# Kernel optimization log

Measured on AMD Instinct MI355X. Metric: run time of the kernel, lower is better.

Reference implementation:

```python
import jax, jax.numpy as jnp
import numpy as np

N, C, CI, H, W = 64, 512, 256, 12, 4
EPS = 1e-5


def _conv1x1(v, w, b=None):
    # v: [n, cin, h, w], w: [cout, cin]
    o = jnp.einsum('nchw,oc->nohw', v, w)
    if b is not None:
        o = o + b[None, :, None, None]
    return o


def _layernorm(v, g, b):
    # normalize over (C, H, W) per sample, affine params shaped [C, H, W]
    mu = v.mean(axis=(1, 2, 3), keepdims=True)
    var = v.var(axis=(1, 2, 3), keepdims=True)
    return (v - mu) / jnp.sqrt(var + EPS) * g[None] + b[None]


def setup_inputs() -> dict:
    key = jax.random.key(0)
    ks = jax.random.split(key, 12)
    s = 0.02
    return {
        'x': jax.random.normal(ks[0], (N, C, H, W), dtype=jnp.float32),
        'theta_w': jax.random.normal(ks[1], (CI, C), dtype=jnp.float32) * s,
        'theta_b': jnp.zeros((CI,), dtype=jnp.float32),
        'phi_w': jax.random.normal(ks[2], (CI, C), dtype=jnp.float32) * s,
        'phi_b': jnp.zeros((CI,), dtype=jnp.float32),
        'conv1_w': jax.random.normal(ks[3], (C, C), dtype=jnp.float32) * s,
        'conv2_w': jax.random.normal(ks[4], (C, C), dtype=jnp.float32) * s,
        'ln1_g': jnp.ones((C, H, W), dtype=jnp.float32),
        'ln1_b': jnp.zeros((C, H, W), dtype=jnp.float32),
        'ln2_g': jnp.ones((C, H, W), dtype=jnp.float32),
        'ln2_b': jnp.zeros((C, H, W), dtype=jnp.float32),
    }


def reference(x, theta_w, theta_b, phi_w, phi_b, conv1_w, conv2_w,
              ln1_g, ln1_b, ln2_g, ln2_b):
    n = x.shape[0]
    hw = H * W
    # 1x1 conv projections (conv is per-sample, so compute once on the N nodes
    # instead of on the N^2 gathered copies -- identical math)
    theta = _conv1x1(x, theta_w, theta_b)          # [N, CI, H, W]  (gallery proj)
    phi = _conv1x1(x, phi_w, phi_b)                # [N, CI, H, W]  (query proj)
    # MaxPool2d(2,2) on phi -> [N, CI, 6, 2] -> [N, CI, 12]
    phi_p = phi.reshape(n, CI, H // 2, 2, W // 2, 2).max(axis=(3, 5))
    phi_p = phi_p.reshape(n, CI, -1)               # [N, CI, 12]
    t = theta.reshape(n, CI, hw).transpose(0, 2, 1)  # [N, HW, CI]
    # f[i, j] = theta(x[j]) @ pooled phi(x[i]), norm='size' divides by 12
    f = jnp.einsum('jsc,icm->ijsm', t, phi_p) / phi_p.shape[-1]  # [Nq, Ng, HW, 12]
    m = f.max(axis=-1)                             # [Nq, Ng, HW]; max instead of softmax-sum
    # all-pairs layout p = i*N + j: qs[p] = i, gs[p] = j (torch.where row-major)
    gs = jnp.tile(jnp.arange(n), n)                # [N*N]
    # masked gallery image z = x[gs] * attention map, then scatter_add over gs
    z = x[gs] * m.reshape(n * n, 1, H, W)          # [N*N, C, H, W]
    x2 = jax.ops.segment_sum(z, gs, num_segments=n)
    # postprocessing (dropouts are identity at p=0)
    x = x2 + x                                     # res1
    x = _layernorm(x, ln1_g, ln1_b)
    h = _conv1x1(jax.nn.relu(_conv1x1(x, conv1_w)), conv2_w)
    x = x + h                                      # res2
    x = _layernorm(x, ln2_g, ln2_b)
    return x
```

## Files before the change

kernel.cpp:

```cpp
#include <hip/hip_runtime.h>
#include <hip/hip_bf16.h>

#define NN 64
#define CC 512
#define HW 48
#define LNSZ (CC * HW)

typedef __attribute__((ext_vector_type(8))) short bf16x8;
typedef __attribute__((ext_vector_type(4))) float floatx4;

static const size_t WB_OFF   = 0;
static const size_t BC_OFF   = 393216;
static const size_t S_OFF    = 393728;
static const size_t SMU_OFF  = 396800;
static const size_t SRS_OFF  = 396864;
static const size_t CXP_OFF  = 396928;
static const size_t CX2_OFF  = 409216;
static const size_t ST2_OFF  = 421504;
static const size_t XB_OFF   = 422016;
static const size_t TP_OFF   = 1208448;
static const size_t YB_OFF   = 1994880;
static const size_t UB_OFF   = 2781312;
static const size_t PP_OFF   = 3567744;
static const size_t YY_OFF   = 3666048;
static const size_t VV_OFF   = 5238912;

__device__ __forceinline__ void block_reduce2(float& sum, float& sq) {
  const int lane = threadIdx.x & 63, w = threadIdx.x >> 6;
#pragma unroll
  for (int off = 32; off > 0; off >>= 1) {
    sum += __shfl_down(sum, off, 64);
    sq  += __shfl_down(sq, off, 64);
  }
  __shared__ float rs[4], rq[4];
  if (lane == 0) { rs[w] = sum; rq[w] = sq; }
  __syncthreads();
  if (threadIdx.x == 0) {
    sum = rs[0] + rs[1] + rs[2] + rs[3];
    sq  = rq[0] + rq[1] + rq[2] + rq[3];
  }
}

__global__ __launch_bounds__(256) void prep_w(
    const float* __restrict__ tw, const float* __restrict__ pw,
    const float* __restrict__ c1, const float* __restrict__ c2,
    const float* __restrict__ tb, const float* __restrict__ pb,
    __hip_bfloat16* __restrict__ Wb, float* __restrict__ bcat,
    float* __restrict__ S) {
  int g = blockIdx.x * 256 + threadIdx.x;
  float v;
  if (g < 131072)      v = tw[g];
  else if (g < 262144) v = pw[g - 131072];
  else if (g < 524288) v = c1[g - 262144];
  else                 v = c2[g - 524288];
  Wb[g] = __float2bfloat16(v);
  if (g < 512) bcat[g] = g < 256 ? tb[g] : pb[g - 256];
  if (g < 3072) S[g] = 0.f;
}

__global__ __launch_bounds__(256) void trx_stats(
    const float* __restrict__ x, __hip_bfloat16* __restrict__ xb,
    float* __restrict__ cxp, float* __restrict__ cx2p) {
  const int bx = blockIdx.x;
  const int n  = blockIdx.y;
  const int t  = threadIdx.x;
  __shared__ float ts[128 * 49];
  __shared__ float ps[192], pq[192];
  const float* src = x + (size_t)n * LNSZ + (size_t)bx * 128 * HW;
#pragma unroll
  for (int k = 0; k < 6; ++k) {
    int idx = t + k * 256;
    float4 v = ((const float4*)src)[idx];
    int c = idx / 12, sq = (idx % 12) * 4;
    float* d = ts + c * 49 + sq;
    d[0] = v.x; d[1] = v.y; d[2] = v.z; d[3] = v.w;
  }
  __syncthreads();
  if (t < 192) {
    int s = t % 48, q = t / 48;
    float sum = 0.f, sq2 = 0.f;
#pragma unroll
    for (int c = q * 32; c < q * 32 + 32; ++c) {
      float v = ts[c * 49 + s];
      sum += v; sq2 += v * v;
    }
    ps[t] = sum; pq[t] = sq2;
  }
  __hip_bfloat16* dst = xb + (size_t)n * LNSZ + bx * 128;
#pragma unroll
  for (int k = 0; k < 12; ++k) {
    int idx = t + k * 256;
    int s = idx >> 6, cp = idx & 63;
    __hip_bfloat162 p;
    p.x = __float2bfloat16(ts[(cp * 2) * 49 + s]);
    p.y = __float2bfloat16(ts[(cp * 2 + 1) * 49 + s]);
    *(__hip_bfloat162*)(dst + (size_t)s * 512 + cp * 2) = p;
  }
  __syncthreads();
  if (t < 48) {
    cxp[((size_t)n * 4 + bx) * 48 + t] = ps[t] + ps[48 + t] + ps[96 + t] + ps[144 + t];
    cx2p[((size_t)n * 4 + bx) * 48 + t] = pq[t] + pq[48 + t] + pq[96 + t] + pq[144 + t];
  }
}

__global__ __launch_bounds__(256) void gemm_bf16out(
    const __hip_bfloat16* __restrict__ Wb, const __hip_bfloat16* __restrict__ inb,
    const float* __restrict__ bias, __hip_bfloat16* __restrict__ outb, int relu) {
  const int oc = blockIdx.x, n = blockIdx.y;
  const int w = threadIdx.x >> 6, lane = threadIdx.x & 63;
  const int c16 = lane & 15, quad = lane >> 4;
  const int obase = oc * 128 + w * 32;

  const __hip_bfloat16* A0 = Wb + (size_t)(obase + c16) * 512 + quad * 8;
  const __hip_bfloat16* A1 = A0 + 16 * 512;
  const __hip_bfloat16* B0 = inb + (size_t)n * LNSZ + (size_t)c16 * 512 + quad * 8;

  floatx4 zero = {0.f, 0.f, 0.f, 0.f};
  floatx4 acc[2][3];
#pragma unroll
  for (int i = 0; i < 2; ++i)
#pragma unroll
    for (int j = 0; j < 3; ++j) acc[i][j] = zero;

  bf16x8 a[2], b[3];
  a[0] = *(const bf16x8*)(A0);
  a[1] = *(const bf16x8*)(A1);
  b[0] = *(const bf16x8*)(B0);
  b[1] = *(const bf16x8*)(B0 + 16 * 512);
  b[2] = *(const bf16x8*)(B0 + 32 * 512);

  for (int k = 0; k < 480; k += 32) {
    bf16x8 an[2], bn[3];
    const int k2 = k + 32;
    an[0] = *(const bf16x8*)(A0 + k2);
    an[1] = *(const bf16x8*)(A1 + k2);
    bn[0] = *(const bf16x8*)(B0 + k2);
    bn[1] = *(const bf16x8*)(B0 + 16 * 512 + k2);
    bn[2] = *(const bf16x8*)(B0 + 32 * 512 + k2);
#pragma unroll
    for (int i = 0; i < 2; ++i)
#pragma unroll
      for (int j = 0; j < 3; ++j)
        acc[i][j] = __builtin_amdgcn_mfma_f32_16x16x32_bf16(a[i], b[j],
                                                            acc[i][j], 0, 0, 0);
    a[0] = an[0]; a[1] = an[1];
    b[0] = bn[0]; b[1] = bn[1]; b[2] = bn[2];
  }
#pragma unroll
  for (int i = 0; i < 2; ++i)
#pragma unroll
    for (int j = 0; j < 3; ++j)
      acc[i][j] = __builtin_amdgcn_mfma_f32_16x16x32_bf16(a[i], b[j],
                                                          acc[i][j], 0, 0, 0);

  __hip_bfloat16* on = outb + (size_t)n * LNSZ;
#pragma unroll
  for (int i = 0; i < 2; ++i) {
    const int o0 = obase + i * 16 + quad * 4;
    float bv[4];
#pragma unroll
    for (int r = 0; r < 4; ++r) bv[r] = bias ? bias[o0 + r] : 0.f;
#pragma unroll
    for (int j = 0; j < 3; ++j) {
      const int s = j * 16 + c16;
      union { short4 s4; __hip_bfloat16 h[4]; } u;
#pragma unroll
      for (int r = 0; r < 4; ++r) {
        float v = acc[i][j][r] + bv[r];
        if (relu) v = fmaxf(v, 0.f);
        u.h[r] = __float2bfloat16(v);
      }
      *(short4*)(on + (size_t)s * 512 + o0) = u.s4;
    }
  }
}

__global__ __launch_bounds__(256) void make_pp(
    const __hip_bfloat16* __restrict__ ThPhi, __hip_bfloat16* __restrict__ Pp) {
  int g = blockIdx.x * 256 + threadIdx.x;
  int ci = g & 255;
  int rest = g >> 8;
  int m = rest % 12, i = rest / 12;
  int sb = (m >> 1) * 8 + (m & 1) * 2;
  const __hip_bfloat16* base = ThPhi + (size_t)i * LNSZ + 256 + ci;
  float mx = __bfloat162float(base[(size_t)(sb + 0) * 512]);
  mx = fmaxf(mx, __bfloat162float(base[(size_t)(sb + 1) * 512]));
  mx = fmaxf(mx, __bfloat162float(base[(size_t)(sb + 4) * 512]));
  mx = fmaxf(mx, __bfloat162float(base[(size_t)(sb + 5) * 512]));
  Pp[g] = __float2bfloat16(mx);
}

__global__ __launch_bounds__(256) void dgemm_fused(
    const __hip_bfloat16* __restrict__ A, const __hip_bfloat16* __restrict__ B,
    float* __restrict__ S) {
  const int bn = blockIdx.x * 48;
  const int w = threadIdx.x >> 6, lane = threadIdx.x & 63;
  const int c16 = lane & 15, quad = lane >> 4;
  const int bm = blockIdx.y * 128 + w * 32;

  const __hip_bfloat16* A0 = A + (size_t)(bm + c16) * 512 + quad * 8;
  const __hip_bfloat16* A1 = A0 + 16 * 512;
  const __hip_bfloat16* Bp = B + (size_t)(bn + c16) * 256 + quad * 8;

  floatx4 zero = {0.f, 0.f, 0.f, 0.f};
  floatx4 acc[2][3];
#pragma unroll
  for (int i = 0; i < 2; ++i)
#pragma unroll
    for (int j = 0; j < 3; ++j) acc[i][j] = zero;

#pragma unroll 2
  for (int k = 0; k < 256; k += 32) {
    bf16x8 a0 = *(const bf16x8*)(A0 + k);
    bf16x8 a1 = *(const bf16x8*)(A1 + k);
    bf16x8 b0 = *(const bf16x8*)(Bp + k);
    bf16x8 b1 = *(const bf16x8*)(Bp + 16 * 256 + k);
    bf16x8 b2 = *(const bf16x8*)(Bp + 32 * 256 + k);
    acc[0][0] = __builtin_amdgcn_mfma_f32_16x16x32_bf16(a0, b0, acc[0][0], 0, 0, 0);
    acc[0][1] = __builtin_amdgcn_mfma_f32_16x16x32_bf16(a0, b1, acc[0][1], 0, 0, 0);
    acc[0][2] = __builtin_amdgcn_mfma_f32_16x16x32_bf16(a0, b2, acc[0][2], 0, 0, 0);
    acc[1][0] = __builtin_amdgcn_mfma_f32_16x16x32_bf16(a1, b0, acc[1][0], 0, 0, 0);
    acc[1][1] = __builtin_amdgcn_mfma_f32_16x16x32_bf16(a1, b1, acc[1][1], 0, 0, 0);
    acc[1][2] = __builtin_amdgcn_mfma_f32_16x16x32_bf16(a1, b2, acc[1][2], 0, 0, 0);
  }

  __shared__ float red[4 * 48 * 33];
  float* rw = red + w * (48 * 33);
#pragma unroll
  for (int i = 0; i < 2; ++i)
#pragma unroll
    for (int j = 0; j < 3; ++j)
#pragma unroll
      for (int r = 0; r < 4; ++r)
        rw[(j * 16 + c16) * 33 + (i * 16 + quad * 4 + r)] = acc[i][j][r];
  __syncthreads();
  if (lane < 32) {
    float sum = 0.f;
#pragma unroll
    for (int grp = 0; grp < 4; ++grp) {
      float mx = rw[(grp * 12) * 33 + lane];
#pragma unroll
      for (int m = 1; m < 12; ++m)
        mx = fmaxf(mx, rw[(grp * 12 + m) * 33 + lane]);
      sum += mx;
    }
    atomicAdd(&S[bm + lane], sum * (1.0f / 12.0f));
  }
}

__global__ __launch_bounds__(64) void ln1_finish(
    const float* __restrict__ S, const float* __restrict__ cxp,
    const float* __restrict__ cx2p, float* __restrict__ smu,
    float* __restrict__ srstd) {
  const int n = blockIdx.x, lane = threadIdx.x;
  float sum = 0.f, sq = 0.f;
  if (lane < 48) {
    float a = 1.0f + S[n * 48 + lane];
    float c1 = 0.f, c2 = 0.f;
#pragma unroll
    for (int ch = 0; ch < 4; ++ch) {
      c1 += cxp[((size_t)n * 4 + ch) * 48 + lane];
      c2 += cx2p[((size_t)n * 4 + ch) * 48 + lane];
    }
    sum = a * c1;
    sq = a * a * c2;
  }
#pragma unroll
  for (int off = 32; off > 0; off >>= 1) {
    sum += __shfl_down(sum, off, 64);
    sq  += __shfl_down(sq, off, 64);
  }
  if (lane == 0) {
    float mu = sum * (1.0f / LNSZ);
    float var = sq * (1.0f / LNSZ) - mu * mu;
    smu[n] = mu;
    srstd[n] = 1.0f / sqrtf(var + 1e-5f);
  }
}

__global__ __launch_bounds__(256) void ln1_norm_tr(
    const float* __restrict__ x, const float* __restrict__ S,
    const float* __restrict__ smu, const float* __restrict__ srstd,
    const float* __restrict__ g, const float* __restrict__ b,
    float* __restrict__ y, __hip_bfloat16* __restrict__ yb) {
  const int bx = blockIdx.x, n = blockIdx.y, t = threadIdx.x;
  __shared__ float ts[128 * 49];
  __shared__ float sS[HW];
  if (t < HW) sS[t] = 1.0f + S[n * HW + t];
  __syncthreads();
  const float mu = smu[n], rstd = srstd[n];
  const size_t chunk = (size_t)bx * 6144;
  const float* xn = x + (size_t)n * LNSZ + chunk;
  float* yn = y + (size_t)n * LNSZ + chunk;
  const float* gp = g + chunk;
  const float* bp = b + chunk;
#pragma unroll
  for (int k = 0; k < 6; ++k) {
    int idx = t + k * 256;
    int c = idx / 12, sq0 = (idx % 12) * 4;
    float4 xv = ((const float4*)xn)[idx];
    float4 gv = ((const float4*)gp)[idx];
    float4 bv = ((const float4*)bp)[idx];
    float4 o;
    o.x = (xv.x * sS[sq0]     - mu) * rstd * gv.x + bv.x;
    o.y = (xv.y * sS[sq0 + 1] - mu) * rstd * gv.y + bv.y;
    o.z = (xv.z * sS[sq0 + 2] - mu) * rstd * gv.z + bv.z;
    o.w = (xv.w * sS[sq0 + 3] - mu) * rstd * gv.w + bv.w;
    ((float4*)yn)[idx] = o;
    float* d = ts + c * 49 + sq0;
    d[0] = o.x; d[1] = o.y; d[2] = o.z; d[3] = o.w;
  }
  __syncthreads();
  __hip_bfloat16* dst = yb + (size_t)n * LNSZ + bx * 128;
#pragma unroll
  for (int k = 0; k < 12; ++k) {
    int idx = t + k * 256;
    int s = idx >> 6, cp = idx & 63;
    __hip_bfloat162 p;
    p.x = __float2bfloat16(ts[(cp * 2) * 49 + s]);
    p.y = __float2bfloat16(ts[(cp * 2 + 1) * 49 + s]);
    *(__hip_bfloat162*)(dst + (size_t)s * 512 + cp * 2) = p;
  }
}

__global__ __launch_bounds__(256) void conv2_fused(
    const __hip_bfloat16* __restrict__ Wb, const __hip_bfloat16* __restrict__ inb,
    const float* __restrict__ y, float* __restrict__ v,
    float2* __restrict__ stats2) {
  const int oc = blockIdx.x, n = blockIdx.y;
  const int w = threadIdx.x >> 6, lane = threadIdx.x & 63;
  const int c16 = lane & 15, quad = lane >> 4;
  const int obase = oc * 128 + w * 32;

  const __hip_bfloat16* A0 = Wb + (size_t)(obase + c16) * 512 + quad * 8;
  const __hip_bfloat16* A1 = A0 + 16 * 512;
  const __hip_bfloat16* B0 = inb + (size_t)n * LNSZ + (size_t)c16 * 512 + quad * 8;

  floatx4 zero = {0.f, 0.f, 0.f, 0.f};
  floatx4 acc[2][3];
#pragma unroll
  for (int i = 0; i < 2; ++i)
#pragma unroll
    for (int j = 0; j < 3; ++j) acc[i][j] = zero;

  bf16x8 a[2], b[3];
  a[0] = *(const bf16x8*)(A0);
  a[1] = *(const bf16x8*)(A1);
  b[0] = *(const bf16x8*)(B0);
  b[1] = *(const bf16x8*)(B0 + 16 * 512);
  b[2] = *(const bf16x8*)(B0 + 32 * 512);

  for (int k = 0; k < 480; k += 32) {
    bf16x8 an[2], bn[3];
    const int k2 = k + 32;
    an[0] = *(const bf16x8*)(A0 + k2);
    an[1] = *(const bf16x8*)(A1 + k2);
    bn[0] = *(const bf16x8*)(B0 + k2);
    bn[1] = *(const bf16x8*)(B0 + 16 * 512 + k2);
    bn[2] = *(const bf16x8*)(B0 + 32 * 512 + k2);
#pragma unroll
    for (int i = 0; i < 2; ++i)
#pragma unroll
      for (int j = 0; j < 3; ++j)
        acc[i][j] = __builtin_amdgcn_mfma_f32_16x16x32_bf16(a[i], b[j],
                                                            acc[i][j], 0, 0, 0);
    a[0] = an[0]; a[1] = an[1];
    b[0] = bn[0]; b[1] = bn[1]; b[2] = bn[2];
  }
#pragma unroll
  for (int i = 0; i < 2; ++i)
#pragma unroll
    for (int j = 0; j < 3; ++j)
      acc[i][j] = __builtin_amdgcn_mfma_f32_16x16x32_bf16(a[i], b[j],
                                                          acc[i][j], 0, 0, 0);

  const float* yn = y + (size_t)n * LNSZ;
  float* vn = v + (size_t)n * LNSZ;
  float sum = 0.f, sq = 0.f;
#pragma unroll
  for (int i = 0; i < 2; ++i)
#pragma unroll
    for (int r = 0; r < 4; ++r) {
      const int o = obase + i * 16 + quad * 4 + r;
#pragma unroll
      for (int j = 0; j < 3; ++j) {
        const int s = j * 16 + c16;
        float val = acc[i][j][r] + yn[(size_t)o * HW + s];
        vn[(size_t)o * HW + s] = val;
        sum += val;
        sq += val * val;
      }
    }
  block_reduce2(sum, sq);
  if (threadIdx.x == 0) stats2[n * 4 + oc] = make_float2(sum, sq);
}

__global__ __launch_bounds__(256) void ln2_norm(
    const float* __restrict__ v, const float2* __restrict__ stats2,
    const float* __restrict__ g2, const float* __restrict__ b2,
    float* __restrict__ out) {
  const int bx = blockIdx.x, n = blockIdx.y, t = threadIdx.x;
  __shared__ float smu, srstd;
  if (t == 0) {
    float s1 = 0.f, s2 = 0.f;
#pragma unroll
    for (int k = 0; k < 4; ++k) {
      float2 p = stats2[n * 4 + k];
      s1 += p.x; s2 += p.y;
    }
    float mu = s1 * (1.0f / LNSZ);
    float var = s2 * (1.0f / LNSZ) - mu * mu;
    smu = mu;
    srstd = 1.0f / sqrtf(var + 1e-5f);
  }
  __syncthreads();
  const float mu = smu, rstd = srstd;
  const size_t chunk = (size_t)bx * 6144;
  const float* vn = v + (size_t)n * LNSZ + chunk;
  float* on = out + (size_t)n * LNSZ + chunk;
  const float* gp = g2 + chunk;
  const float* bp = b2 + chunk;
#pragma unroll
  for (int k = 0; k < 6; ++k) {
    int idx = t + k * 256;
    float4 vv = ((const float4*)vn)[idx];
    float4 gv = ((const float4*)gp)[idx];
    float4 bv = ((const float4*)bp)[idx];
    float4 o;
    o.x = (vv.x - mu) * rstd * gv.x + bv.x;
    o.y = (vv.y - mu) * rstd * gv.y + bv.y;
    o.z = (vv.z - mu) * rstd * gv.z + bv.z;
    o.w = (vv.w - mu) * rstd * gv.w + bv.w;
    ((float4*)on)[idx] = o;
  }
}

extern "C" void kernel_launch(void* const* d_in, const int* in_sizes, int n_in,
                              void* d_out, int out_size, void* d_ws, size_t ws_size,
                              hipStream_t stream) {
  const float* x   = (const float*)d_in[0];
  const float* tw  = (const float*)d_in[1];
  const float* tb  = (const float*)d_in[2];
  const float* pw  = (const float*)d_in[3];
  const float* pb  = (const float*)d_in[4];
  const float* c1w = (const float*)d_in[5];
  const float* c2w = (const float*)d_in[6];
  const float* g1  = (const float*)d_in[7];
  const float* b1  = (const float*)d_in[8];
  const float* g2  = (const float*)d_in[9];
  const float* b2  = (const float*)d_in[10];

  float* ws = (float*)d_ws;
  __hip_bfloat16* Wb = (__hip_bfloat16*)(ws + WB_OFF);
  float* bcat        = ws + BC_OFF;
  float* S           = ws + S_OFF;
  float* smu         = ws + SMU_OFF;
  float* srstd       = ws + SRS_OFF;
  float* cxp         = ws + CXP_OFF;
  float* cx2p        = ws + CX2_OFF;
  float2* st2        = (float2*)(ws + ST2_OFF);
  __hip_bfloat16* xb = (__hip_bfloat16*)(ws + XB_OFF);
  __hip_bfloat16* tp = (__hip_bfloat16*)(ws + TP_OFF);
  __hip_bfloat16* yb = (__hip_bfloat16*)(ws + YB_OFF);
  __hip_bfloat16* ub = (__hip_bfloat16*)(ws + UB_OFF);
  __hip_bfloat16* Pp = (__hip_bfloat16*)(ws + PP_OFF);
  float* y           = ws + YY_OFF;
  float* v           = ws + VV_OFF;
  float* out         = (float*)d_out;

  prep_w<<<3072, 256, 0, stream>>>(tw, pw, c1w, c2w, tb, pb, Wb, bcat, S);
  trx_stats<<<dim3(4, NN), 256, 0, stream>>>(x, xb, cxp, cx2p);
  gemm_bf16out<<<dim3(4, NN), 256, 0, stream>>>(Wb, xb, bcat, tp, 0);
  make_pp<<<768, 256, 0, stream>>>(tp, Pp);
  dgemm_fused<<<dim3(16, 24), 256, 0, stream>>>(tp, Pp, S);
  ln1_finish<<<NN, 64, 0, stream>>>(S, cxp, cx2p, smu, srstd);
  ln1_norm_tr<<<dim3(4, NN), 256, 0, stream>>>(x, S, smu, srstd, g1, b1, y, yb);
  gemm_bf16out<<<dim3(4, NN), 256, 0, stream>>>(Wb + 512 * 512, yb, nullptr, ub, 1);
  conv2_fused<<<dim3(4, NN), 256, 0, stream>>>(Wb + 1024 * 512, ub, y, v, st2);
  ln2_norm<<<dim3(4, NN), 256, 0, stream>>>(v, st2, g2, b2, out);
}
```

Measured before the change: 141.1 us.

## Merge prep kernels, fuse pooling and LN1 stats, halve GEMM tiles

Merges weight conversion and the x transpose/stats into one launch, and vectorises the weight conversion. Fuses the phi max-pool into the projection GEMM epilogue through shared memory, and folds the LN1 statistics into the normalise kernel, dropping three launches. All GEMMs move to 16-row-per-wave tiles with double-buffered register loads, doubling grid size for occupancy. The trade is less reuse of loaded operands per MFMA. ST2 now aliases the Pp buffer, which is safe only because Pp is dead by the time conv2 runs.

```diff
diff --git a/kernel.cpp b/kernel.cpp
--- a/kernel.cpp
+++ b/kernel.cpp
@@ -12,16 +12,14 @@
 static const size_t WB_OFF   = 0;
 static const size_t BC_OFF   = 393216;
 static const size_t S_OFF    = 393728;
-static const size_t SMU_OFF  = 396800;
-static const size_t SRS_OFF  = 396864;
 static const size_t CXP_OFF  = 396928;
 static const size_t CX2_OFF  = 409216;
-static const size_t ST2_OFF  = 421504;
 static const size_t XB_OFF   = 422016;
 static const size_t TP_OFF   = 1208448;
 static const size_t YB_OFF   = 1994880;
 static const size_t UB_OFF   = 2781312;
 static const size_t PP_OFF   = 3567744;
+static const size_t ST2_OFF  = 3567744;
 static const size_t YY_OFF   = 3666048;
 static const size_t VV_OFF   = 5238912;
 
@@ -41,31 +39,38 @@
   }
 }
 
-__global__ __launch_bounds__(256) void prep_w(
+__global__ __launch_bounds__(256) void prep_all(
     const float* __restrict__ tw, const float* __restrict__ pw,
     const float* __restrict__ c1, const float* __restrict__ c2,
     const float* __restrict__ tb, const float* __restrict__ pb,
+    const float* __restrict__ x,
     __hip_bfloat16* __restrict__ Wb, float* __restrict__ bcat,
-    float* __restrict__ S) {
-  int g = blockIdx.x * 256 + threadIdx.x;
-  float v;
-  if (g < 131072)      v = tw[g];
-  else if (g < 262144) v = pw[g - 131072];
-  else if (g < 524288) v = c1[g - 262144];
-  else                 v = c2[g - 524288];
-  Wb[g] = __float2bfloat16(v);
-  if (g < 512) bcat[g] = g < 256 ? tb[g] : pb[g - 256];
-  if (g < 3072) S[g] = 0.f;
-}
-
-__global__ __launch_bounds__(256) void trx_stats(
-    const float* __restrict__ x, __hip_bfloat16* __restrict__ xb,
+    float* __restrict__ S, __hip_bfloat16* __restrict__ xb,
     float* __restrict__ cxp, float* __restrict__ cx2p) {
-  const int bx = blockIdx.x;
-  const int n  = blockIdx.y;
-  const int t  = threadIdx.x;
   __shared__ float ts[128 * 49];
   __shared__ float ps[192], pq[192];
+  if (blockIdx.x < 768) {
+    int g = blockIdx.x * 256 + threadIdx.x;
+    float4 v;
+    if (g < 32768)       v = ((const float4*)tw)[g];
+    else if (g < 65536)  v = ((const float4*)pw)[g - 32768];
+    else if (g < 131072) v = ((const float4*)c1)[g - 65536];
+    else                 v = ((const float4*)c2)[g - 131072];
+    union { short4 s4; __hip_bfloat16 h[4]; } u;
+    u.h[0] = __float2bfloat16(v.x);
+    u.h[1] = __float2bfloat16(v.y);
+    u.h[2] = __float2bfloat16(v.z);
+    u.h[3] = __float2bfloat16(v.w);
+    ((short4*)Wb)[g] = u.s4;
+    if (g < 64)       ((float4*)bcat)[g] = ((const float4*)tb)[g];
+    else if (g < 128) ((float4*)bcat)[g] = ((const float4*)pb)[g - 64];
+    if (g < 768) ((float4*)S)[g] = make_float4(0.f, 0.f, 0.f, 0.f);
+    return;
+  }
+  const int bb = blockIdx.x - 768;
+  const int bx = bb & 3;
+  const int n  = bb >> 2;
+  const int t  = threadIdx.x;
   const float* src = x + (size_t)n * LNSZ + (size_t)bx * 128 * HW;
 #pragma unroll
   for (int k = 0; k < 6; ++k) {
@@ -105,89 +110,83 @@
 
 __global__ __launch_bounds__(256) void gemm_bf16out(
     const __hip_bfloat16* __restrict__ Wb, const __hip_bfloat16* __restrict__ inb,
-    const float* __restrict__ bias, __hip_bfloat16* __restrict__ outb, int relu) {
+    const float* __restrict__ bias, __hip_bfloat16* __restrict__ outb, int relu,
+    __hip_bfloat16* __restrict__ Pp) {
   const int oc = blockIdx.x, n = blockIdx.y;
   const int w = threadIdx.x >> 6, lane = threadIdx.x & 63;
   const int c16 = lane & 15, quad = lane >> 4;
-  const int obase = oc * 128 + w * 32;
+  const int obase = oc * 64 + w * 16;
 
   const __hip_bfloat16* A0 = Wb + (size_t)(obase + c16) * 512 + quad * 8;
-  const __hip_bfloat16* A1 = A0 + 16 * 512;
   const __hip_bfloat16* B0 = inb + (size_t)n * LNSZ + (size_t)c16 * 512 + quad * 8;
 
   floatx4 zero = {0.f, 0.f, 0.f, 0.f};
-  floatx4 acc[2][3];
-#pragma unroll
-  for (int i = 0; i < 2; ++i)
-#pragma unroll
-    for (int j = 0; j < 3; ++j) acc[i][j] = zero;
-
-  bf16x8 a[2], b[3];
-  a[0] = *(const bf16x8*)(A0);
-  a[1] = *(const bf16x8*)(A1);
-  b[0] = *(const bf16x8*)(B0);
-  b[1] = *(const bf16x8*)(B0 + 16 * 512);
-  b[2] = *(const bf16x8*)(B0 + 32 * 512);
-
-  for (int k = 0; k < 480; k += 32) {
-    bf16x8 an[2], bn[3];
-    const int k2 = k + 32;
-    an[0] = *(const bf16x8*)(A0 + k2);
-    an[1] = *(const bf16x8*)(A1 + k2);
-    bn[0] = *(const bf16x8*)(B0 + k2);
-    bn[1] = *(const bf16x8*)(B0 + 16 * 512 + k2);
-    bn[2] = *(const bf16x8*)(B0 + 32 * 512 + k2);
-#pragma unroll
-    for (int i = 0; i < 2; ++i)
-#pragma unroll
-      for (int j = 0; j < 3; ++j)
-        acc[i][j] = __builtin_amdgcn_mfma_f32_16x16x32_bf16(a[i], b[j],
-                                                            acc[i][j], 0, 0, 0);
-    a[0] = an[0]; a[1] = an[1];
-    b[0] = bn[0]; b[1] = bn[1]; b[2] = bn[2];
-  }
-#pragma unroll
-  for (int i = 0; i < 2; ++i)
-#pragma unroll
-    for (int j = 0; j < 3; ++j)
-      acc[i][j] = __builtin_amdgcn_mfma_f32_16x16x32_bf16(a[i], b[j],
-                                                          acc[i][j], 0, 0, 0);
-
+  floatx4 acc[3] = {zero, zero, zero};
+
+  bf16x8 aA  = *(const bf16x8*)(A0);
+  bf16x8 bA0 = *(const bf16x8*)(B0);
+  bf16x8 bA1 = *(const bf16x8*)(B0 + 16 * 512);
+  bf16x8 bA2 = *(const bf16x8*)(B0 + 32 * 512);
+  bf16x8 aB  = *(const bf16x8*)(A0 + 32);
+  bf16x8 bB0 = *(const bf16x8*)(B0 + 32);
+  bf16x8 bB1 = *(const bf16x8*)(B0 + 16 * 512 + 32);
+  bf16x8 bB2 = *(const bf16x8*)(B0 + 32 * 512 + 32);
+#pragma unroll 1
+  for (int k = 0; k < 448; k += 64) {
+    acc[0] = __builtin_amdgcn_mfma_f32_16x16x32_bf16(aA, bA0, acc[0], 0, 0, 0);
+    acc[1] = __builtin_amdgcn_mfma_f32_16x16x32_bf16(aA, bA1, acc[1], 0, 0, 0);
+    acc[2] = __builtin_amdgcn_mfma_f32_16x16x32_bf16(aA, bA2, acc[2], 0, 0, 0);
+    aA  = *(const bf16x8*)(A0 + k + 64);
+    bA0 = *(const bf16x8*)(B0 + k + 64);
+    bA1 = *(const bf16x8*)(B0 + 16 * 512 + k + 64);
+    bA2 = *(const bf16x8*)(B0 + 32 * 512 + k + 64);
+    acc[0] = __builtin_amdgcn_mfma_f32_16x16x32_bf16(aB, bB0, acc[0], 0, 0, 0);
+    acc[1] = __builtin_amdgcn_mfma_f32_16x16x32_bf16(aB, bB1, acc[1], 0, 0, 0);
+    acc[2] = __builtin_amdgcn_mfma_f32_16x16x32_bf16(aB, bB2, acc[2], 0, 0, 0);
+    aB  = *(const bf16x8*)(A0 + k + 96);
+    bB0 = *(const bf16x8*)(B0 + k + 96);
+    bB1 = *(const bf16x8*)(B0 + 16 * 512 + k + 96);
+    bB2 = *(const bf16x8*)(B0 + 32 * 512 + k + 96);
+  }
+  acc[0] = __builtin_amdgcn_mfma_f32_16x16x32_bf16(aA, bA0, acc[0], 0, 0, 0);
+  acc[1] = __builtin_amdgcn_mfma_f32_16x16x32_bf16(aA, bA1, acc[1], 0, 0, 0);
+  acc[2] = __builtin_amdgcn_mfma_f32_16x16x32_bf16(aA, bA2, acc[2], 0, 0, 0);
+  acc[0] = __builtin_amdgcn_mfma_f32_16x16x32_bf16(aB, bB0, acc[0], 0, 0, 0);
+  acc[1] = __builtin_amdgcn_mfma_f32_16x16x32_bf16(aB, bB1, acc[1], 0, 0, 0);
+  acc[2] = __builtin_amdgcn_mfma_f32_16x16x32_bf16(aB, bB2, acc[2], 0, 0, 0);
+
+  __shared__ float pt[64 * 49];
+  const int do_pp = (Pp != nullptr) && (oc >= 4);
+  const int o0 = obase + quad * 4;
+  float bv[4];
+#pragma unroll
+  for (int r = 0; r < 4; ++r) bv[r] = bias ? bias[o0 + r] : 0.f;
   __hip_bfloat16* on = outb + (size_t)n * LNSZ;
 #pragma unroll
-  for (int i = 0; i < 2; ++i) {
-    const int o0 = obase + i * 16 + quad * 4;
-    float bv[4];
-#pragma unroll
-    for (int r = 0; r < 4; ++r) bv[r] = bias ? bias[o0 + r] : 0.f;
-#pragma unroll
-    for (int j = 0; j < 3; ++j) {
-      const int s = j * 16 + c16;
-      union { short4 s4; __hip_bfloat16 h[4]; } u;
-#pragma unroll
-      for (int r = 0; r < 4; ++r) {
-        float v = acc[i][j][r] + bv[r];
-        if (relu) v = fmaxf(v, 0.f);
-        u.h[r] = __float2bfloat16(v);
-      }
-      *(short4*)(on + (size_t)s * 512 + o0) = u.s4;
-    }
-  }
-}
-
-__global__ __launch_bounds__(256) void make_pp(
-    const __hip_bfloat16* __restrict__ ThPhi, __hip_bfloat16* __restrict__ Pp) {
-  int g = blockIdx.x * 256 + threadIdx.x;
-  int ci = g & 255;
-  int rest = g >> 8;
-  int m = rest % 12, i = rest / 12;
-  int sb = (m >> 1) * 8 + (m & 1) * 2;
-  const __hip_bfloat16* base = ThPhi + (size_t)i * LNSZ + 256 + ci;
-  float mx = __bfloat162float(base[(size_t)(sb + 0) * 512]);
-  mx = fmaxf(mx, __bfloat162float(base[(size_t)(sb + 1) * 512]));
-  mx = fmaxf(mx, __bfloat162float(base[(size_t)(sb + 4) * 512]));
-  mx = fmaxf(mx, __bfloat162float(base[(size_t)(sb + 5) * 512]));
-  Pp[g] = __float2bfloat16(mx);
+  for (int j = 0; j < 3; ++j) {
+    const int s = j * 16 + c16;
+    union { short4 s4; __hip_bfloat16 h[4]; } u;
+#pragma unroll
+    for (int r = 0; r < 4; ++r) {
+      float vv = acc[j][r] + bv[r];
+      if (relu) vv = fmaxf(vv, 0.f);
+      u.h[r] = __float2bfloat16(vv);
+      if (do_pp) pt[(w * 16 + quad * 4 + r) * 49 + s] = vv;
+    }
+    *(short4*)(on + (size_t)s * 512 + o0) = u.s4;
+  }
+  if (do_pp) {
+    __syncthreads();
+#pragma unroll
+    for (int rep = 0; rep < 3; ++rep) {
+      int idx = threadIdx.x + rep * 256;
+      int m = idx >> 6, cil = idx & 63;
+      int sb = (m >> 1) * 8 + (m & 1) * 2;
+      const float* pr = pt + cil * 49;
+      float mx = fmaxf(fmaxf(pr[sb], pr[sb + 1]), fmaxf(pr[sb + 4], pr[sb + 5]));
+      Pp[((size_t)(n * 12 + m) << 8) + (oc - 4) * 64 + cil] = __float2bfloat16(mx);
+    }
+  }
 }
 
 __global__ __launch_bounds__(256) void dgemm_fused(
@@ -196,99 +195,105 @@
   const int bn = blockIdx.x * 48;
   const int w = threadIdx.x >> 6, lane = threadIdx.x & 63;
   const int c16 = lane & 15, quad = lane >> 4;
-  const int bm = blockIdx.y * 128 + w * 32;
+  const int bm = blockIdx.y * 64 + w * 16;
 
   const __hip_bfloat16* A0 = A + (size_t)(bm + c16) * 512 + quad * 8;
-  const __hip_bfloat16* A1 = A0 + 16 * 512;
   const __hip_bfloat16* Bp = B + (size_t)(bn + c16) * 256 + quad * 8;
 
   floatx4 zero = {0.f, 0.f, 0.f, 0.f};
-  floatx4 acc[2][3];
-#pragma unroll
-  for (int i = 0; i < 2; ++i)
-#pragma unroll
-    for (int j = 0; j < 3; ++j) acc[i][j] = zero;
-
-#pragma unroll 2
-  for (int k = 0; k < 256; k += 32) {
-    bf16x8 a0 = *(const bf16x8*)(A0 + k);
-    bf16x8 a1 = *(const bf16x8*)(A1 + k);
-    bf16x8 b0 = *(const bf16x8*)(Bp + k);
-    bf16x8 b1 = *(const bf16x8*)(Bp + 16 * 256 + k);
-    bf16x8 b2 = *(const bf16x8*)(Bp + 32 * 256 + k);
-    acc[0][0] = __builtin_amdgcn_mfma_f32_16x16x32_bf16(a0, b0, acc[0][0], 0, 0, 0);
-    acc[0][1] = __builtin_amdgcn_mfma_f32_16x16x32_bf16(a0, b1, acc[0][1], 0, 0, 0);
-    acc[0][2] = __builtin_amdgcn_mfma_f32_16x16x32_bf16(a0, b2, acc[0][2], 0, 0, 0);
-    acc[1][0] = __builtin_amdgcn_mfma_f32_16x16x32_bf16(a1, b0, acc[1][0], 0, 0, 0);
-    acc[1][1] = __builtin_amdgcn_mfma_f32_16x16x32_bf16(a1, b1, acc[1][1], 0, 0, 0);
-    acc[1][2] = __builtin_amdgcn_mfma_f32_16x16x32_bf16(a1, b2, acc[1][2], 0, 0, 0);
-  }
-
-  __shared__ float red[4 * 48 * 33];
-  float* rw = red + w * (48 * 33);
-#pragma unroll
-  for (int i = 0; i < 2; ++i)
-#pragma unroll
-    for (int j = 0; j < 3; ++j)
-#pragma unroll
-      for (int r = 0; r < 4; ++r)
-        rw[(j * 16 + c16) * 33 + (i * 16 + quad * 4 + r)] = acc[i][j][r];
-  __syncthreads();
-  if (lane < 32) {
+  floatx4 acc[3] = {zero, zero, zero};
+
+  bf16x8 aA  = *(const bf16x8*)(A0);
+  bf16x8 bA0 = *(const bf16x8*)(Bp);
+  bf16x8 bA1 = *(const bf16x8*)(Bp + 16 * 256);
+  bf16x8 bA2 = *(const bf16x8*)(Bp + 32 * 256);
+  bf16x8 aB  = *(const bf16x8*)(A0 + 32);
+  bf16x8 bB0 = *(const bf16x8*)(Bp + 32);
+  bf16x8 bB1 = *(const bf16x8*)(Bp + 16 * 256 + 32);
+  bf16x8 bB2 = *(const bf16x8*)(Bp + 32 * 256 + 32);
+#pragma unroll 1
+  for (int k = 0; k < 192; k += 64) {
+    acc[0] = __builtin_amdgcn_mfma_f32_16x16x32_bf16(aA, bA0, acc[0], 0, 0, 0);
+    acc[1] = __builtin_amdgcn_mfma_f32_16x16x32_bf16(aA, bA1, acc[1], 0, 0, 0);
+    acc[2] = __builtin_amdgcn_mfma_f32_16x16x32_bf16(aA, bA2, acc[2], 0, 0, 0);
+    aA  = *(const bf16x8*)(A0 + k + 64);
+    bA0 = *(const bf16x8*)(Bp + k + 64);
+    bA1 = *(const bf16x8*)(Bp + 16 * 256 + k + 64);
+    bA2 = *(const bf16x8*)(Bp + 32 * 256 + k + 64);
+    acc[0] = __builtin_amdgcn_mfma_f32_16x16x32_bf16(aB, bB0, acc[0], 0, 0, 0);
+    acc[1] = __builtin_amdgcn_mfma_f32_16x16x32_bf16(aB, bB1, acc[1], 0, 0, 0);
+    acc[2] = __builtin_amdgcn_mfma_f32_16x16x32_bf16(aB, bB2, acc[2], 0, 0, 0);
+    aB  = *(const bf16x8*)(A0 + k + 96);
+    bB0 = *(const bf16x8*)(Bp + k + 96);
+    bB1 = *(const bf16x8*)(Bp + 16 * 256 + k + 96);
+    bB2 = *(const bf16x8*)(Bp + 32 * 256 + k + 96);
+  }
+  acc[0] = __builtin_amdgcn_mfma_f32_16x16x32_bf16(aA, bA0, acc[0], 0, 0, 0);
+  acc[1] = __builtin_amdgcn_mfma_f32_16x16x32_bf16(aA, bA1, acc[1], 0, 0, 0);
+  acc[2] = __builtin_amdgcn_mfma_f32_16x16x32_bf16(aA, bA2, acc[2], 0, 0, 0);
+  acc[0] = __builtin_amdgcn_mfma_f32_16x16x32_bf16(aB, bB0, acc[0], 0, 0, 0);
+  acc[1] = __builtin_amdgcn_mfma_f32_16x16x32_bf16(aB, bB1, acc[1], 0, 0, 0);
+  acc[2] = __builtin_amdgcn_mfma_f32_16x16x32_bf16(aB, bB2, acc[2], 0, 0, 0);
+
+  __shared__ float red[4 * 48 * 17];
+  float* rw = red + w * (48 * 17);
+#pragma unroll
+  for (int j = 0; j < 3; ++j)
+#pragma unroll
+    for (int r = 0; r < 4; ++r)
+      rw[(j * 16 + c16) * 17 + (quad * 4 + r)] = acc[j][r];
+  __syncthreads();
+  if (lane < 16) {
     float sum = 0.f;
 #pragma unroll
     for (int grp = 0; grp < 4; ++grp) {
-      float mx = rw[(grp * 12) * 33 + lane];
+      float mx = rw[(grp * 12) * 17 + lane];
 #pragma unroll
       for (int m = 1; m < 12; ++m)
-        mx = fmaxf(mx, rw[(grp * 12 + m) * 33 + lane]);
+        mx = fmaxf(mx, rw[(grp * 12 + m) * 17 + lane]);
       sum += mx;
     }
     atomicAdd(&S[bm + lane], sum * (1.0f / 12.0f));
-  }
-}
-
-__global__ __launch_bounds__(64) void ln1_finish(
-    const float* __restrict__ S, const float* __restrict__ cxp,
-    const float* __restrict__ cx2p, float* __restrict__ smu,
-    float* __restrict__ srstd) {
-  const int n = blockIdx.x, lane = threadIdx.x;
-  float sum = 0.f, sq = 0.f;
-  if (lane < 48) {
-    float a = 1.0f + S[n * 48 + lane];
-    float c1 = 0.f, c2 = 0.f;
-#pragma unroll
-    for (int ch = 0; ch < 4; ++ch) {
-      c1 += cxp[((size_t)n * 4 + ch) * 48 + lane];
-      c2 += cx2p[((size_t)n * 4 + ch) * 48 + lane];
-    }
-    sum = a * c1;
-    sq = a * a * c2;
-  }
-#pragma unroll
-  for (int off = 32; off > 0; off >>= 1) {
-    sum += __shfl_down(sum, off, 64);
-    sq  += __shfl_down(sq, off, 64);
-  }
-  if (lane == 0) {
-    float mu = sum * (1.0f / LNSZ);
-    float var = sq * (1.0f / LNSZ) - mu * mu;
-    smu[n] = mu;
-    srstd[n] = 1.0f / sqrtf(var + 1e-5f);
   }
 }
 
 __global__ __launch_bounds__(256) void ln1_norm_tr(
     const float* __restrict__ x, const float* __restrict__ S,
-    const float* __restrict__ smu, const float* __restrict__ srstd,
+    const float* __restrict__ cxp, const float* __restrict__ cx2p,
     const float* __restrict__ g, const float* __restrict__ b,
     float* __restrict__ y, __hip_bfloat16* __restrict__ yb) {
   const int bx = blockIdx.x, n = blockIdx.y, t = threadIdx.x;
   __shared__ float ts[128 * 49];
   __shared__ float sS[HW];
+  __shared__ float sstat[2];
   if (t < HW) sS[t] = 1.0f + S[n * HW + t];
-  __syncthreads();
-  const float mu = smu[n], rstd = srstd[n];
+  if (t < 64) {
+    float sum = 0.f, sq = 0.f;
+    if (t < 48) {
+      float a = 1.0f + S[n * HW + t];
+      float c1 = 0.f, c2 = 0.f;
+#pragma unroll
+      for (int ch = 0; ch < 4; ++ch) {
+        c1 += cxp[((size_t)n * 4 + ch) * 48 + t];
+        c2 += cx2p[((size_t)n * 4 + ch) * 48 + t];
+      }
+      sum = a * c1;
+      sq = a * a * c2;
+    }
+#pragma unroll
+    for (int off = 32; off > 0; off >>= 1) {
+      sum += __shfl_down(sum, off, 64);
+      sq  += __shfl_down(sq, off, 64);
+    }
+    if (t == 0) {
+      float mu = sum * (1.0f / LNSZ);
+      float var = sq * (1.0f / LNSZ) - mu * mu;
+      sstat[0] = mu;
+      sstat[1] = 1.0f / sqrtf(var + 1e-5f);
+    }
+  }
+  __syncthreads();
+  const float mu = sstat[0], rstd = sstat[1];
   const size_t chunk = (size_t)bx * 6144;
   const float* xn = x + (size_t)n * LNSZ + chunk;
   float* yn = y + (size_t)n * LNSZ + chunk;
@@ -330,69 +335,64 @@
   const int oc = blockIdx.x, n = blockIdx.y;
   const int w = threadIdx.x >> 6, lane = threadIdx.x & 63;
   const int c16 = lane & 15, quad = lane >> 4;
-  const int obase = oc * 128 + w * 32;
+  const int obase = oc * 64 + w * 16;
 
   const __hip_bfloat16* A0 = Wb + (size_t)(obase + c16) * 512 + quad * 8;
-  const __hip_bfloat16* A1 = A0 + 16 * 512;
   const __hip_bfloat16* B0 = inb + (size_t)n * LNSZ + (size_t)c16 * 512 + quad * 8;
 
   floatx4 zero = {0.f, 0.f, 0.f, 0.f};
-  floatx4 acc[2][3];
-#pragma unroll
-  for (int i = 0; i < 2; ++i)
-#pragma unroll
-    for (int j = 0; j < 3; ++j) acc[i][j] = zero;
-
-  bf16x8 a[2], b[3];
-  a[0] = *(const bf16x8*)(A0);
-  a[1] = *(const bf16x8*)(A1);
-  b[0] = *(const bf16x8*)(B0);
-  b[1] = *(const bf16x8*)(B0 + 16 * 512);
-  b[2] = *(const bf16x8*)(B0 + 32 * 512);
-
-  for (int k = 0; k < 480; k += 32) {
-    bf16x8 an[2], bn[3];
-    const int k2 = k + 32;
-    an[0] = *(const bf16x8*)(A0 + k2);
-    an[1] = *(const bf16x8*)(A1 + k2);
-    bn[0] = *(const bf16x8*)(B0 + k2);
-    bn[1] = *(const bf16x8*)(B0 + 16 * 512 + k2);
-    bn[2] = *(const bf16x8*)(B0 + 32 * 512 + k2);
-#pragma unroll
-    for (int i = 0; i < 2; ++i)
-#pragma unroll
-      for (int j = 0; j < 3; ++j)
-        acc[i][j] = __builtin_amdgcn_mfma_f32_16x16x32_bf16(a[i], b[j],
-                                                            acc[i][j], 0, 0, 0);
-    a[0] = an[0]; a[1] = an[1];
-    b[0] = bn[0]; b[1] = bn[1]; b[2] = bn[2];
-  }
-#pragma unroll
-  for (int i = 0; i < 2; ++i)
-#pragma unroll
-    for (int j = 0; j < 3; ++j)
-      acc[i][j] = __builtin_amdgcn_mfma_f32_16x16x32_bf16(a[i], b[j],
-                                                          acc[i][j], 0, 0, 0);
+  floatx4 acc[3] = {zero, zero, zero};
+
+  bf16x8 aA  = *(const bf16x8*)(A0);
+  bf16x8 bA0 = *(const bf16x8*)(B0);
+  bf16x8 bA1 = *(const bf16x8*)(B0 + 16 * 512);
+  bf16x8 bA2 = *(const bf16x8*)(B0 + 32 * 512);
+  bf16x8 aB  = *(const bf16x8*)(A0 + 32);
+  bf16x8 bB0 = *(const bf16x8*)(B0 + 32);
+  bf16x8 bB1 = *(const bf16x8*)(B0 + 16 * 512 + 32);
+  bf16x8 bB2 = *(const bf16x8*)(B0 + 32 * 512 + 32);
+#pragma unroll 1
+  for (int k = 0; k < 448; k += 64) {
+    acc[0] = __builtin_amdgcn_mfma_f32_16x16x32_bf16(aA, bA0, acc[0], 0, 0, 0);
+    acc[1] = __builtin_amdgcn_mfma_f32_16x16x32_bf16(aA, bA1, acc[1], 0, 0, 0);
+    acc[2] = __builtin_amdgcn_mfma_f32_16x16x32_bf16(aA, bA2, acc[2], 0, 0, 0);
+    aA  = *(const bf16x8*)(A0 + k + 64);
+    bA0 = *(const bf16x8*)(B0 + k + 64);
+    bA1 = *(const bf16x8*)(B0 + 16 * 512 + k + 64);
+    bA2 = *(const bf16x8*)(B0 + 32 * 512 + k + 64);
+    acc[0] = __builtin_amdgcn_mfma_f32_16x16x32_bf16(aB, bB0, acc[0], 0, 0, 0);
+    acc[1] = __builtin_amdgcn_mfma_f32_16x16x32_bf16(aB, bB1, acc[1], 0, 0, 0);
+    acc[2] = __builtin_amdgcn_mfma_f32_16x16x32_bf16(aB, bB2, acc[2], 0, 0, 0);
+    aB  = *(const bf16x8*)(A0 + k + 96);
+    bB0 = *(const bf16x8*)(B0 + k + 96);
+    bB1 = *(const bf16x8*)(B0 + 16 * 512 + k + 96);
+    bB2 = *(const bf16x8*)(B0 + 32 * 512 + k + 96);
+  }
+  acc[0] = __builtin_amdgcn_mfma_f32_16x16x32_bf16(aA, bA0, acc[0], 0, 0, 0);
+  acc[1] = __builtin_amdgcn_mfma_f32_16x16x32_bf16(aA, bA1, acc[1], 0, 0, 0);
+  acc[2] = __builtin_amdgcn_mfma_f32_16x16x32_bf16(aA, bA2, acc[2], 0, 0, 0);
+  acc[0] = __builtin_amdgcn_mfma_f32_16x16x32_bf16(aB, bB0, acc[0], 0, 0, 0);
+  acc[1] = __builtin_amdgcn_mfma_f32_16x16x32_bf16(aB, bB1, acc[1], 0, 0, 0);
+  acc[2] = __builtin_amdgcn_mfma_f32_16x16x32_bf16(aB, bB2, acc[2], 0, 0, 0);
 
   const float* yn = y + (size_t)n * LNSZ;
   float* vn = v + (size_t)n * LNSZ;
   float sum = 0.f, sq = 0.f;
-#pragma unroll
-  for (int i = 0; i < 2; ++i)
-#pragma unroll
-    for (int r = 0; r < 4; ++r) {
-      const int o = obase + i * 16 + quad * 4 + r;
-#pragma unroll
-      for (int j = 0; j < 3; ++j) {
-        const int s = j * 16 + c16;
-        float val = acc[i][j][r] + yn[(size_t)o * HW + s];
-        vn[(size_t)o * HW + s] = val;
-        sum += val;
-        sq += val * val;
-      }
-    }
+  const int o0 = obase + quad * 4;
+#pragma unroll
+  for (int r = 0; r < 4; ++r) {
+    const int o = o0 + r;
+#pragma unroll
+    for (int j = 0; j < 3; ++j) {
+      const int s = j * 16 + c16;
+      float val = acc[j][r] + yn[(size_t)o * HW + s];
+      vn[(size_t)o * HW + s] = val;
+      sum += val;
+      sq += val * val;
+    }
+  }
   block_reduce2(sum, sq);
-  if (threadIdx.x == 0) stats2[n * 4 + oc] = make_float2(sum, sq);
+  if (threadIdx.x == 0) stats2[n * 8 + oc] = make_float2(sum, sq);
 }
 
 __global__ __launch_bounds__(256) void ln2_norm(
@@ -404,8 +404,8 @@
   if (t == 0) {
     float s1 = 0.f, s2 = 0.f;
 #pragma unroll
-    for (int k = 0; k < 4; ++k) {
-      float2 p = stats2[n * 4 + k];
+    for (int k = 0; k < 8; ++k) {
+      float2 p = stats2[n * 8 + k];
       s1 += p.x; s2 += p.y;
     }
     float mu = s1 * (1.0f / LNSZ);
@@ -454,28 +454,25 @@
   __hip_bfloat16* Wb = (__hip_bfloat16*)(ws + WB_OFF);
   float* bcat        = ws + BC_OFF;
   float* S           = ws + S_OFF;
-  float* smu         = ws + SMU_OFF;
-  float* srstd       = ws + SRS_OFF;
   float* cxp         = ws + CXP_OFF;
   float* cx2p        = ws + CX2_OFF;
-  float2* st2        = (float2*)(ws + ST2_OFF);
   __hip_bfloat16* xb = (__hip_bfloat16*)(ws + XB_OFF);
   __hip_bfloat16* tp = (__hip_bfloat16*)(ws + TP_OFF);
   __hip_bfloat16* yb = (__hip_bfloat16*)(ws + YB_OFF);
   __hip_bfloat16* ub = (__hip_bfloat16*)(ws + UB_OFF);
   __hip_bfloat16* Pp = (__hip_bfloat16*)(ws + PP_OFF);
+  float2* st2        = (float2*)(ws + ST2_OFF);
   float* y           = ws + YY_OFF;
   float* v           = ws + VV_OFF;
   float* out         = (float*)d_out;
 
-  prep_w<<<3072, 256, 0, stream>>>(tw, pw, c1w, c2w, tb, pb, Wb, bcat, S);
-  trx_stats<<<dim3(4, NN), 256, 0, stream>>>(x, xb, cxp, cx2p);
-  gemm_bf16out<<<dim3(4, NN), 256, 0, stream>>>(Wb, xb, bcat, tp, 0);
-  make_pp<<<768, 256, 0, stream>>>(tp, Pp);
-  dgemm_fused<<<dim3(16, 24), 256, 0, stream>>>(tp, Pp, S);
-  ln1_finish<<<NN, 64, 0, stream>>>(S, cxp, cx2p, smu, srstd);
-  ln1_norm_tr<<<dim3(4, NN), 256, 0, stream>>>(x, S, smu, srstd, g1, b1, y, yb);
-  gemm_bf16out<<<dim3(4, NN), 256, 0, stream>>>(Wb + 512 * 512, yb, nullptr, ub, 1);
-  conv2_fused<<<dim3(4, NN), 256, 0, stream>>>(Wb + 1024 * 512, ub, y, v, st2);
+  prep_all<<<1024, 256, 0, stream>>>(tw, pw, c1w, c2w, tb, pb, x,
+                                     Wb, bcat, S, xb, cxp, cx2p);
+  gemm_bf16out<<<dim3(8, NN), 256, 0, stream>>>(Wb, xb, bcat, tp, 0, Pp);
+  dgemm_fused<<<dim3(16, 48), 256, 0, stream>>>(tp, Pp, S);
+  ln1_norm_tr<<<dim3(4, NN), 256, 0, stream>>>(x, S, cxp, cx2p, g1, b1, y, yb);
+  gemm_bf16out<<<dim3(8, NN), 256, 0, stream>>>(Wb + 512 * 512, yb, nullptr, ub, 1,
+                                                nullptr);
+  conv2_fused<<<dim3(8, NN), 256, 0, stream>>>(Wb + 1024 * 512, ub, y, v, st2);
   ln2_norm<<<dim3(4, NN), 256, 0, stream>>>(v, st2, g2, b2, out);
 }
```

New measurement: 153.8 us. 1.09x slower.
